# Optimization experiments

Measured on AMD Instinct MI355X. Metric: run time of the kernel, lower is better.

The kernel has to match this reference:

```python
import jax, jax.numpy as jnp
import numpy as np

B, N, DIM, H = 4, 2048, 256, 8
HD = DIM // H  # head_dim = 32
N_LAYERS = 2


def quantum_map(x):
    # cat over last dim: [cos(x+i*pi/2), sin(x+i*pi/2)] for i in 0..n_layers-1
    feats = []
    for i in range(N_LAYERS):
        phase = x + i * (np.pi / 2)
        feats.append(jnp.cos(phase))
        feats.append(jnp.sin(phase))
    return jnp.concatenate(feats, axis=-1)  # [..., 4*HD]


def setup_inputs() -> dict:
    key = jax.random.key(0)
    ks = jax.random.split(key, 10)
    s = 1.0 / np.sqrt(DIM)
    return {
        "x": jax.random.normal(ks[0], (B, N, DIM), dtype=jnp.float32),
        "topo_weights": jax.random.uniform(ks[1], (B, N, N), dtype=jnp.float32),
        "Wq": jax.random.normal(ks[2], (DIM, DIM), dtype=jnp.float32) * s,
        "bq": jnp.zeros((DIM,), jnp.float32),
        "Wk": jax.random.normal(ks[3], (DIM, DIM), dtype=jnp.float32) * s,
        "bk": jnp.zeros((DIM,), jnp.float32),
        "Wv": jax.random.normal(ks[4], (DIM, DIM), dtype=jnp.float32) * s,
        "bv": jnp.zeros((DIM,), jnp.float32),
        "Wo": jax.random.normal(ks[5], (DIM, DIM), dtype=jnp.float32) * s,
        "bo": jnp.zeros((DIM,), jnp.float32),
    }


def reference(x, topo_weights, Wq, bq, Wk, bk, Wv, bv, Wo, bo):
    b, n, c = x.shape
    q = (x @ Wq + bq).reshape(b, n, H, HD)
    k = (x @ Wk + bk).reshape(b, n, H, HD)
    v = (x @ Wv + bv).reshape(b, n, H, HD)
    q = quantum_map(q)  # [b,n,H,4*HD]
    k = quantum_map(k)
    scores = jnp.einsum('bnhd,bmhd->bnmh', q, k) / np.sqrt(HD)
    scores = scores * topo_weights[..., None]  # [b,n,m,h]
    attn = jax.nn.softmax(scores, axis=2)
    out = jnp.einsum('bnmh,bmhd->bnhd', attn, v).reshape(b, n, c)
    return out @ Wo + bo
```

## Files before the change

### kernel.cpp

```cpp
#include <hip/hip_runtime.h>
#include <math.h>

#define Bn 4
#define Nn 2048
#define Hn 8
#define HDn 32
#define Dn 256
#define MHALF 1024
#define NT 64

typedef _Float16 h1;
typedef __attribute__((ext_vector_type(2))) _Float16 h2;
typedef __attribute__((ext_vector_type(2))) __fp16 g2;
typedef __attribute__((ext_vector_type(8))) _Float16 h8;
typedef __attribute__((ext_vector_type(4))) float fx4;

#define QSCALE 0.35355339059327373f
#define QS_L2E 0.5101185553493001f
#define SH_L2E 5.770780163555851f

__global__ __launch_bounds__(256) void cvtW_kernel(
    const float* __restrict__ Wq, const float* __restrict__ Wk,
    const float* __restrict__ Wv, h1* __restrict__ WT)
{
    __shared__ float tw[64][65];
    const int w = blockIdx.z;
    const int d0 = blockIdx.y * 64, o0 = blockIdx.x * 64;
    const float* W = (w == 0) ? Wq : (w == 1) ? Wk : Wv;
    const int rr = threadIdx.x >> 6, cc = threadIdx.x & 63;
#pragma unroll
    for (int i = 0; i < 16; ++i)
        tw[rr + i * 4][cc] = W[(size_t)(d0 + rr + i * 4) * 256 + o0 + cc];
    __syncthreads();
#pragma unroll
    for (int i = 0; i < 16; ++i) {
        const int row = rr + i * 4;
        WT[(size_t)w * 65536 + (size_t)(o0 + row) * 256 + d0 + cc] = (h1)tw[cc][row];
    }
}

__global__ __launch_bounds__(256) __attribute__((amdgpu_waves_per_eu(4, 4)))
void proj_kernel(
    const float* __restrict__ x, const h1* __restrict__ WT,
    const float* __restrict__ bq, const float* __restrict__ bk,
    const float* __restrict__ bv,
    h1* __restrict__ fq, h1* __restrict__ fk, h1* __restrict__ vT)
{
    __shared__ __align__(16) h1 fbuf[64][264];
    const int tid = threadIdx.x;
    const int w = tid >> 6;
    const int lane = tid & 63;
    const int quad = lane >> 4;
    const int l15 = lane & 15;
    const int wsel = blockIdx.y >> 1;
    const int hg = blockIdx.y & 1;
    const int r0 = blockIdx.x * 64;
    const int arow = r0 + w * 16 + l15;
    const int b = r0 >> 11, n0 = r0 & (Nn - 1);

    const h1* WTw = WT + (size_t)wsel * 65536;
    fx4 acc[8];
#pragma unroll
    for (int ct = 0; ct < 8; ++ct) acc[ct] = (fx4){0.f, 0.f, 0.f, 0.f};

    for (int ks = 0; ks < 8; ++ks) {
        float xv[8];
        *(float4*)&xv[0] = *(const float4*)&x[(size_t)arow * 256 + ks * 32 + quad * 8];
        *(float4*)&xv[4] = *(const float4*)&x[(size_t)arow * 256 + ks * 32 + quad * 8 + 4];
        h8 Ahi, Alo;
#pragma unroll
        for (int j = 0; j < 8; ++j) {
            const h1 hi = (h1)xv[j];
            Ahi[j] = hi;
            Alo[j] = (h1)(xv[j] - (float)hi);
        }
        h8 Bf[8];
#pragma unroll
        for (int ct = 0; ct < 8; ++ct)
            Bf[ct] = *(const h8*)&WTw[(size_t)(hg * 128 + ct * 16 + l15) * 256 + ks * 32 + quad * 8];
#pragma unroll
        for (int ct = 0; ct < 8; ++ct) {
            acc[ct] = __builtin_amdgcn_mfma_f32_16x16x32_f16(Ahi, Bf[ct], acc[ct], 0, 0, 0);
            acc[ct] = __builtin_amdgcn_mfma_f32_16x16x32_f16(Alo, Bf[ct], acc[ct], 0, 0, 0);
        }
    }

    const float* bias = (wsel == 0) ? bq : (wsel == 1) ? bk : bv;

    if (wsel < 2) {
        h1* f = (wsel == 0) ? fq : fk;
#pragma unroll
        for (int ct = 0; ct < 8; ++ct) {
            const int c = ct * 16 + l15;
            const float bb = bias[hg * 128 + c];
            const int hh4 = c >> 5, dd = c & 31;
#pragma unroll
            for (int r = 0; r < 4; ++r) {
                const float val = acc[ct][r] + bb;
                const float sv = __sinf(val), cv = __cosf(val);
                h1* fp = &fbuf[w * 16 + quad * 4 + r][hh4 * 64 + dd];
                fp[0]  = (h1)cv;
                fp[32] = (h1)sv;
            }
        }
        __syncthreads();
        const int row = tid >> 2, q4 = tid & 3;
#pragma unroll
        for (int g = 0; g < 8; ++g) {
            const int chunk = q4 + g * 4;
            const int hh4 = chunk >> 3, within = chunk & 7;
            const h8 val = *(const h8*)&fbuf[row][hh4 * 64 + within * 8];
            const int head = hg * 4 + hh4;
            *(h8*)&f[((size_t)(b * Hn + head) * Nn + n0 + row) * 64 + within * 8] = val;
        }
    } else {
        h1 (*vst)[132] = (h1(*)[132])fbuf;
#pragma unroll
        for (int ct = 0; ct < 8; ++ct) {
            const int c = ct * 16 + l15;
            const float bb = bias[hg * 128 + c];
#pragma unroll
            for (int r = 0; r < 4; ++r)
                vst[w * 16 + quad * 4 + r][c] = (h1)(acc[ct][r] + bb);
        }
        __syncthreads();
        const int c2 = tid & 127, half = tid >> 7;
        const int head = hg * 4 + (c2 >> 5), dd = c2 & 31;
        h1* vp = vT + ((size_t)((b * Hn + head) * HDn + dd)) * Nn + n0;
#pragma unroll
        for (int g = 0; g < 4; ++g) {
            const int gg = half * 4 + g;
            h8 pk;
#pragma unroll
            for (int j = 0; j < 8; ++j) {
                const int zz = gg * 8 + j;
                const int blk = zz >> 5, z = zz & 31;
                const int src = blk * 32 + ((z & 7) >> 2) * 16 + (z >> 3) * 4 + (z & 3);
                pk[j] = vst[src][c2];
            }
            *(h8*)(vp + gg * 8) = pk;
        }
    }
}

__global__ __launch_bounds__(512, 1) void attn_kernel(
    const h1* __restrict__ fq, const h1* __restrict__ fk, const h1* __restrict__ vT,
    const float* __restrict__ topo, float* __restrict__ pacc, float* __restrict__ pl)
{
    __shared__ __align__(16) float tbuf[2][NT][40];

    const int b = blockIdx.y;
    const int mh = blockIdx.z;
    const int n0 = blockIdx.x * NT;
    const int tid = threadIdx.x;
    const int w = tid >> 6;
    const int h = w;
    const int lane = tid & 63;
    const int quad = lane >> 4;
    const int l15 = lane & 15;

    const h1* qfh = fq + (size_t)(b * Hn + h) * Nn * 64;
    const h1* kfh = fk + (size_t)(b * Hn + h) * Nn * 64;
    const h1* vTh = vT + (size_t)(b * Hn + h) * HDn * Nn;

    const int trow = tid >> 3, tcol4 = (tid & 7) * 4;
    const float* tpg = topo + (size_t)b * Nn * Nn + (size_t)(n0 + trow) * Nn + tcol4;

    h8 qfr[4][2];
#pragma unroll
    for (int qs = 0; qs < 4; ++qs)
#pragma unroll
        for (int ks = 0; ks < 2; ++ks)
            qfr[qs][ks] = *(const h8*)(qfh + (size_t)(n0 + qs * 16 + l15) * 64 + ks * 32 + quad * 8);

    fx4 acc[4][2];
    float lsum[4];
#pragma unroll
    for (int qs = 0; qs < 4; ++qs) {
#pragma unroll
        for (int ds = 0; ds < 2; ++ds) acc[qs][ds] = (fx4){0.f, 0.f, 0.f, 0.f};
        lsum[qs] = 0.f;
    }

    const int mbase = mh * MHALF;
    const fx4 z4 = {0.f, 0.f, 0.f, 0.f};

    float4 rt = *(const float4*)(tpg + mbase);

    for (int it = 0; it < MHALF / 32; ++it) {
        const int m0 = mbase + it * 32;
        const int cur = it & 1;

        h8 kfr[2][2];
#pragma unroll
        for (int ms = 0; ms < 2; ++ms)
#pragma unroll
            for (int ks = 0; ks < 2; ++ks)
                kfr[ms][ks] = *(const h8*)(kfh + (size_t)(m0 + ms * 16 + l15) * 64 + ks * 32 + quad * 8);
        h8 bV[2];
#pragma unroll
        for (int ds = 0; ds < 2; ++ds)
            bV[ds] = *(const h8*)(vTh + (size_t)(ds * 16 + l15) * Nn + m0 + quad * 8);

        *(float4*)&tbuf[cur][trow][tcol4] = rt;
        if (it < MHALF / 32 - 1) rt = *(const float4*)(tpg + m0 + 32);
        __asm__ volatile("s_waitcnt lgkmcnt(0)\n\ts_barrier" ::: "memory");

#pragma unroll
        for (int qs = 0; qs < 4; ++qs) {
            h2 pk[2][2];
#pragma unroll
            for (int ms = 0; ms < 2; ++ms) {
                fx4 tmp = __builtin_amdgcn_mfma_f32_16x16x32_f16(kfr[ms][0], qfr[qs][0], z4, 0, 0, 0);
                fx4 S2  = __builtin_amdgcn_mfma_f32_16x16x32_f16(kfr[ms][1], qfr[qs][1], tmp, 0, 0, 0);
                const fx4 tv = *(const fx4*)&tbuf[cur][qs * 16 + l15][ms * 16 + quad * 4];
                const float p0 = exp2f(fmaf(S2[0] * tv[0], QS_L2E, -SH_L2E));
                const float p1 = exp2f(fmaf(S2[1] * tv[1], QS_L2E, -SH_L2E));
                const float p2 = exp2f(fmaf(S2[2] * tv[2], QS_L2E, -SH_L2E));
                const float p3 = exp2f(fmaf(S2[3] * tv[3], QS_L2E, -SH_L2E));
                lsum[qs] += (p0 + p1) + (p2 + p3);
                pk[ms][0] = __builtin_bit_cast(h2, __builtin_amdgcn_cvt_pkrtz(p0, p1));
                pk[ms][1] = __builtin_bit_cast(h2, __builtin_amdgcn_cvt_pkrtz(p2, p3));
            }
            union { h8 v; h2 p[4]; } pa;
            pa.p[0] = pk[0][0]; pa.p[1] = pk[0][1];
            pa.p[2] = pk[1][0]; pa.p[3] = pk[1][1];
#pragma unroll
            for (int ds = 0; ds < 2; ++ds)
                acc[qs][ds] = __builtin_amdgcn_mfma_f32_16x16x32_f16(pa.v, bV[ds], acc[qs][ds], 0, 0, 0);
        }
    }

#pragma unroll
    for (int qs = 0; qs < 4; ++qs) {
        lsum[qs] += __shfl_xor(lsum[qs], 16);
        lsum[qs] += __shfl_xor(lsum[qs], 32);
    }

    float* paccm = pacc + (size_t)mh * Bn * Nn * Dn;
    float* plm   = pl   + (size_t)mh * Bn * Nn * Hn;
#pragma unroll
    for (int qs = 0; qs < 4; ++qs) {
#pragma unroll
        for (int r = 0; r < 4; ++r) {
            const size_t grow = (size_t)b * Nn + n0 + qs * 16 + quad * 4 + r;
            paccm[grow * Dn + h * HDn + l15]      = acc[qs][0][r];
            paccm[grow * Dn + h * HDn + 16 + l15] = acc[qs][1][r];
        }
        if (quad == 0)
            plm[((size_t)b * Nn + n0 + qs * 16 + l15) * Hn + h] = lsum[qs];
    }
}

__global__ __launch_bounds__(256) void oproj_kernel(
    const float* __restrict__ pacc, const float* __restrict__ pl,
    const float* __restrict__ Wo, const float* __restrict__ bo,
    float* __restrict__ out)
{
    __shared__ float ysT[256][12];
    const int t = threadIdx.x;
    const int r0 = blockIdx.x * 8;
    const int h = t >> 5;
    const size_t PACC = (size_t)Bn * Nn * Dn;
    const size_t PL = (size_t)Bn * Nn * Hn;
#pragma unroll
    for (int i = 0; i < 8; ++i) {
        const size_t row = (size_t)(r0 + i);
        float l = 0.f, yv = 0.f;
#pragma unroll
        for (int m = 0; m < 2; ++m) {
            l  += pl[m * PL + row * Hn + h];
            yv += pacc[m * PACC + row * Dn + t];
        }
        ysT[t][i] = yv * __builtin_amdgcn_rcpf(l);
    }
    __syncthreads();

    float acc8[8];
#pragma unroll
    for (int i = 0; i < 8; ++i) acc8[i] = 0.f;
#pragma unroll 4
    for (int d = 0; d < 256; ++d) {
        const float wv = Wo[d * 256 + t];
        float yy[8];
        *(float4*)&yy[0] = *(const float4*)&ysT[d][0];
        *(float4*)&yy[4] = *(const float4*)&ysT[d][4];
#pragma unroll
        for (int i = 0; i < 8; ++i) acc8[i] = fmaf(yy[i], wv, acc8[i]);
    }
    const float bb = bo[t];
#pragma unroll
    for (int i = 0; i < 8; ++i)
        out[(size_t)(r0 + i) * 256 + t] = acc8[i] + bb;
}

extern "C" void kernel_launch(void* const* d_in, const int* in_sizes, int n_in,
                              void* d_out, int out_size, void* d_ws, size_t ws_size,
                              hipStream_t stream)
{
    const float* x    = (const float*)d_in[0];
    const float* topo = (const float*)d_in[1];
    const float* Wq   = (const float*)d_in[2];
    const float* bq   = (const float*)d_in[3];
    const float* Wk   = (const float*)d_in[4];
    const float* bk   = (const float*)d_in[5];
    const float* Wv   = (const float*)d_in[6];
    const float* bv   = (const float*)d_in[7];
    const float* Wo   = (const float*)d_in[8];
    const float* bo   = (const float*)d_in[9];
    float* out = (float*)d_out;

    char* ws = (char*)d_ws;
    const size_t MB = 1024 * 1024;
    h1* WT = (h1*)ws;
    h1* fq = (h1*)(ws + 1 * MB);
    h1* fk = (h1*)(ws + 9 * MB);
    h1* vT = (h1*)(ws + 17 * MB);
    float* pacc = (float*)(ws + 21 * MB);
    float* pl   = (float*)(ws + 37 * MB);

    cvtW_kernel<<<dim3(4, 4, 3), 256, 0, stream>>>(Wq, Wk, Wv, WT);
    proj_kernel<<<dim3(128, 6), 256, 0, stream>>>(x, WT, bq, bk, bv, fq, fk, vT);
    attn_kernel<<<dim3(Nn / NT, Bn, 2), 512, 0, stream>>>(fq, fk, vT, topo, pacc, pl);
    oproj_kernel<<<(Bn * Nn) / 8, 256, 0, stream>>>(pacc, pl, Wo, bo, out);
}
```

Before: 232.4 us.

## Move output projection onto MFMA with fp16 hi/lo split of activations

The output projection changes from scalar FP32 FMAs over an LDS-staged tile to MFMA 16x16x32 fp16 instructions. Wo is transposed and converted to fp16 by the existing weight conversion kernel. The activations are split into fp16 high and low parts to keep accuracy close to FP32, which costs two MFMAs per tile. The weights themselves are rounded to fp16, which adds some error to the output.

```diff
diff --git a/kernel.cpp b/kernel.cpp
--- a/kernel.cpp
+++ b/kernel.cpp
@@ -11,7 +11,6 @@
 
 typedef _Float16 h1;
 typedef __attribute__((ext_vector_type(2))) _Float16 h2;
-typedef __attribute__((ext_vector_type(2))) __fp16 g2;
 typedef __attribute__((ext_vector_type(8))) _Float16 h8;
 typedef __attribute__((ext_vector_type(4))) float fx4;
 
@@ -21,12 +20,13 @@
 
 __global__ __launch_bounds__(256) void cvtW_kernel(
     const float* __restrict__ Wq, const float* __restrict__ Wk,
-    const float* __restrict__ Wv, h1* __restrict__ WT)
+    const float* __restrict__ Wv, const float* __restrict__ Wo,
+    h1* __restrict__ WT)
 {
     __shared__ float tw[64][65];
     const int w = blockIdx.z;
     const int d0 = blockIdx.y * 64, o0 = blockIdx.x * 64;
-    const float* W = (w == 0) ? Wq : (w == 1) ? Wk : Wv;
+    const float* W = (w == 0) ? Wq : (w == 1) ? Wk : (w == 2) ? Wv : Wo;
     const int rr = threadIdx.x >> 6, cc = threadIdx.x & 63;
 #pragma unroll
     for (int i = 0; i < 16; ++i)
@@ -254,44 +254,65 @@
 
 __global__ __launch_bounds__(256) void oproj_kernel(
     const float* __restrict__ pacc, const float* __restrict__ pl,
-    const float* __restrict__ Wo, const float* __restrict__ bo,
+    const h1* __restrict__ WoT, const float* __restrict__ bo,
     float* __restrict__ out)
 {
-    __shared__ float ysT[256][12];
-    const int t = threadIdx.x;
-    const int r0 = blockIdx.x * 8;
-    const int h = t >> 5;
+    const int tid = threadIdx.x;
+    const int w = tid >> 6;
+    const int lane = tid & 63;
+    const int quad = lane >> 4;
+    const int l15 = lane & 15;
+    const int r0 = blockIdx.x * 64;
+    const int hg = blockIdx.y;
+    const int arow = r0 + w * 16 + l15;
     const size_t PACC = (size_t)Bn * Nn * Dn;
     const size_t PL = (size_t)Bn * Nn * Hn;
-#pragma unroll
-    for (int i = 0; i < 8; ++i) {
-        const size_t row = (size_t)(r0 + i);
-        float l = 0.f, yv = 0.f;
-#pragma unroll
-        for (int m = 0; m < 2; ++m) {
-            l  += pl[m * PL + row * Hn + h];
-            yv += pacc[m * PACC + row * Dn + t];
-        }
-        ysT[t][i] = yv * __builtin_amdgcn_rcpf(l);
-    }
-    __syncthreads();
-
-    float acc8[8];
-#pragma unroll
-    for (int i = 0; i < 8; ++i) acc8[i] = 0.f;
-#pragma unroll 4
-    for (int d = 0; d < 256; ++d) {
-        const float wv = Wo[d * 256 + t];
-        float yy[8];
-        *(float4*)&yy[0] = *(const float4*)&ysT[d][0];
-        *(float4*)&yy[4] = *(const float4*)&ysT[d][4];
-#pragma unroll
-        for (int i = 0; i < 8; ++i) acc8[i] = fmaf(yy[i], wv, acc8[i]);
-    }
-    const float bb = bo[t];
-#pragma unroll
-    for (int i = 0; i < 8; ++i)
-        out[(size_t)(r0 + i) * 256 + t] = acc8[i] + bb;
+
+    float rl[8];
+#pragma unroll
+    for (int hh = 0; hh < 8; ++hh) {
+        const float l = pl[(size_t)arow * Hn + hh] + pl[PL + (size_t)arow * Hn + hh];
+        rl[hh] = __builtin_amdgcn_rcpf(l);
+    }
+
+    fx4 acc[8];
+#pragma unroll
+    for (int ct = 0; ct < 8; ++ct) acc[ct] = (fx4){0.f, 0.f, 0.f, 0.f};
+
+    for (int ks = 0; ks < 8; ++ks) {
+        float a0[8], a1[8];
+        const size_t base = (size_t)arow * Dn + ks * 32 + quad * 8;
+        *(float4*)&a0[0] = *(const float4*)&pacc[base];
+        *(float4*)&a0[4] = *(const float4*)&pacc[base + 4];
+        *(float4*)&a1[0] = *(const float4*)&pacc[PACC + base];
+        *(float4*)&a1[4] = *(const float4*)&pacc[PACC + base + 4];
+        h8 Ahi, Alo;
+#pragma unroll
+        for (int j = 0; j < 8; ++j) {
+            const float yv = (a0[j] + a1[j]) * rl[ks];
+            const h1 hi = (h1)yv;
+            Ahi[j] = hi;
+            Alo[j] = (h1)(yv - (float)hi);
+        }
+        h8 Bf[8];
+#pragma unroll
+        for (int ct = 0; ct < 8; ++ct)
+            Bf[ct] = *(const h8*)&WoT[(size_t)(hg * 128 + ct * 16 + l15) * 256 + ks * 32 + quad * 8];
+#pragma unroll
+        for (int ct = 0; ct < 8; ++ct) {
+            acc[ct] = __builtin_amdgcn_mfma_f32_16x16x32_f16(Ahi, Bf[ct], acc[ct], 0, 0, 0);
+            acc[ct] = __builtin_amdgcn_mfma_f32_16x16x32_f16(Alo, Bf[ct], acc[ct], 0, 0, 0);
+        }
+    }
+
+#pragma unroll
+    for (int ct = 0; ct < 8; ++ct) {
+        const int col = hg * 128 + ct * 16 + l15;
+        const float bb = bo[col];
+#pragma unroll
+        for (int r = 0; r < 4; ++r)
+            out[(size_t)(r0 + w * 16 + quad * 4 + r) * 256 + col] = acc[ct][r] + bb;
+    }
 }
 
 extern "C" void kernel_launch(void* const* d_in, const int* in_sizes, int n_in,
@@ -319,8 +340,8 @@
     float* pacc = (float*)(ws + 21 * MB);
     float* pl   = (float*)(ws + 37 * MB);
 
-    cvtW_kernel<<<dim3(4, 4, 3), 256, 0, stream>>>(Wq, Wk, Wv, WT);
+    cvtW_kernel<<<dim3(4, 4, 4), 256, 0, stream>>>(Wq, Wk, Wv, Wo, WT);
     proj_kernel<<<dim3(128, 6), 256, 0, stream>>>(x, WT, bq, bk, bv, fq, fk, vT);
     attn_kernel<<<dim3(Nn / NT, Bn, 2), 512, 0, stream>>>(fq, fk, vT, topo, pacc, pl);
-    oproj_kernel<<<(Bn * Nn) / 8, 256, 0, stream>>>(pacc, pl, Wo, bo, out);
-}
+    oproj_kernel<<<dim3(128, 2), 256, 0, stream>>>(pacc, pl, WT + 3 * 65536, bo, out);
+}
```

Measured after the change: 212.9 us. -8.4%, faster.
